# Kernel tuning notes

Hardware: AMD Instinct MI355X
Metric: run time of the kernel (lower is better)

The kernel has to match this reference:

```python
import jax, jax.numpy as jnp
import numpy as np
import math

B, L, IN, HID, NLAYERS, AA = 16, 512, 512, 512, 6, 21
KAPPA_ADD = 5.0


def _sru_layer(x, W, v, b):
    # x: [L, B, din]; W: [din, 2*HID*k]; v, b: [2(gate f/r), 2(dir), HID]
    Lx, Bx, din = x.shape
    d = HID
    k = W.shape[1] // (2 * d)  # 4 if projecting residual, 3 if residual = input
    U = (x @ W).reshape(Lx, Bx, 2, d, k)
    res = U[..., 3] if k == 4 else x.reshape(Lx, Bx, 2, d)
    # time-flip direction 1 so a single scan handles both directions
    flip = lambda a: jnp.concatenate([a[:, :, :1], a[::-1, :, 1:]], axis=2)
    u0, u1, u2, resf = flip(U[..., 0]), flip(U[..., 1]), flip(U[..., 2]), flip(res)
    vf, vr = v[0], v[1]
    bf, br = b[0], b[1]

    def step(c, t):
        u0t, u1t, u2t, rt = t
        f = jax.nn.sigmoid(u1t + vf * c + bf)
        c1 = f * c + (1.0 - f) * u0t
        r = jax.nn.sigmoid(u2t + vr * c1 + br)
        h = r * c1 + (1.0 - r) * rt
        return c1, h

    c0 = jnp.zeros((Bx, 2, d), x.dtype)
    _, H = jax.lax.scan(step, c0, (u0, u1, u2, resf))
    return flip(H).reshape(Lx, Bx, 2 * d)


def setup_inputs():
    key = jax.random.key(0)
    inp = {}
    inp['input'] = jax.random.normal(jax.random.fold_in(key, 0), (B, L, IN), jnp.float32)
    inp['hidden'] = jnp.zeros((NLAYERS, B, 2 * HID), jnp.float32)
    for l in range(NLAYERS):
        din = IN if l == 0 else 2 * HID
        k = 4 if din != 2 * HID else 3
        inp[f'sru_w{l}'] = jax.random.normal(jax.random.fold_in(key, 10 + l), (din, 2 * HID * k), jnp.float32) * (1.0 / math.sqrt(din))
        inp[f'sru_v{l}'] = jax.random.normal(jax.random.fold_in(key, 20 + l), (2, 2, HID), jnp.float32) * 0.1
        inp[f'sru_b{l}'] = jnp.zeros((2, 2, HID), jnp.float32)

    def lin(seed, din, dout):
        w = jax.random.normal(jax.random.fold_in(key, seed), (din, dout), jnp.float32) * (1.0 / math.sqrt(din))
        return w, jnp.zeros((dout,), jnp.float32)

    inp['fc1_logits_w'], inp['fc1_logits_b'] = lin(30, 2 * HID, HID)
    inp['fc2_logits_w'], inp['fc2_logits_b'] = lin(31, HID, AA)
    inp['fc1_angles_w'], inp['fc1_angles_b'] = lin(32, 2 * HID, HID)
    inp['fc2_means_w'], inp['fc2_means_b'] = lin(33, HID, 2)
    inp['fc2_kappas_w'], inp['fc2_kappas_b'] = lin(34, HID, 2)
    return inp


def reference(input, hidden, sru_w0, sru_v0, sru_b0, sru_w1, sru_v1, sru_b1, sru_w2, sru_v2, sru_b2, sru_w3, sru_v3, sru_b3, sru_w4, sru_v4, sru_b4, sru_w5, sru_v5, sru_b5, fc1_logits_w, fc1_logits_b, fc2_logits_w, fc2_logits_b, fc1_angles_w, fc1_angles_b, fc2_means_w, fc2_means_b, fc2_kappas_w, fc2_kappas_b):
    x = input.transpose(1, 0, 2)  # [L, B, IN]
    ws = [sru_w0, sru_w1, sru_w2, sru_w3, sru_w4, sru_w5]
    vs = [sru_v0, sru_v1, sru_v2, sru_v3, sru_v4, sru_v5]
    bs = [sru_b0, sru_b1, sru_b2, sru_b3, sru_b4, sru_b5]
    for W, v, b in zip(ws, vs, bs):
        x = _sru_layer(x, W, v, b)
    sru_out = x.transpose(1, 0, 2)  # [B, L, 2*HID]
    h_log = sru_out @ fc1_logits_w + fc1_logits_b
    output_logits = jax.nn.log_softmax(h_log @ fc2_logits_w + fc2_logits_b, axis=-1)
    h_ang = sru_out @ fc1_angles_w + fc1_angles_b
    output_means = jnp.tanh(h_ang @ fc2_means_w + fc2_means_b) * math.pi
    output_kappas = KAPPA_ADD + jax.nn.softplus(h_ang @ fc2_kappas_w + fc2_kappas_b)
    return (output_logits, output_means, output_kappas)
```

## Files before the change

kernel.cpp:

```cpp
#include <hip/hip_runtime.h>

typedef __attribute__((ext_vector_type(8))) short short8;
typedef __attribute__((ext_vector_type(4))) float f32x4;

__device__ __forceinline__ ushort f2bf(float x) {
  unsigned u = __builtin_bit_cast(unsigned, x);
  u = (u + 0x7fffu + ((u >> 16) & 1u)) >> 16;
  return (ushort)u;
}
__device__ __forceinline__ float bf2f(ushort x) {
  return __builtin_bit_cast(float, ((unsigned)x) << 16);
}

#define AS1CP(p) ((const __attribute__((address_space(1))) unsigned int*)(p))
#define AS3CP(p) ((__attribute__((address_space(3))) unsigned int*)(p))
#define GLDS(g, l, SZ) __builtin_amdgcn_global_load_lds(AS1CP(g), AS3CP(l), SZ, 0, 0)

__global__ __launch_bounds__(256) void k_cvt(const float* __restrict__ in,
                                             ushort* __restrict__ out, int n4) {
  int i = blockIdx.x * 256 + threadIdx.x;
  if (i >= n4) return;
  float4 v = reinterpret_cast<const float4*>(in)[i];
  ushort4 o;
  o.x = f2bf(v.x); o.y = f2bf(v.y); o.z = f2bf(v.z); o.w = f2bf(v.w);
  reinterpret_cast<ushort4*>(out)[i] = o;
}

__global__ __launch_bounds__(256) void k_transpose(const float* __restrict__ W,
                                                   ushort* __restrict__ Wt,
                                                   int N, int K) {
  __shared__ float tile[32][33];
  int bx = blockIdx.x * 32;
  int by = blockIdx.y * 32;
  int tx = threadIdx.x, ty = threadIdx.y;
#pragma unroll
  for (int i = 0; i < 32; i += 8)
    tile[ty + i][tx] = W[(size_t)(by + ty + i) * N + bx + tx];
  __syncthreads();
#pragma unroll
  for (int i = 0; i < 32; i += 8)
    Wt[(size_t)(bx + ty + i) * K + by + tx] = f2bf(tile[tx][ty + i]);
}

template <int KKp>
__global__ __launch_bounds__(256) void k_transpose_sru(const float* __restrict__ W,
                                                       ushort* __restrict__ Wt,
                                                       int N, int K) {
  __shared__ float tile[32][33];
  int bx = blockIdx.x * 32;
  int by = blockIdx.y * 32;
  int tx = threadIdx.x, ty = threadIdx.y;
#pragma unroll
  for (int i = 0; i < 32; i += 8)
    tile[ty + i][tx] = W[(size_t)(by + ty + i) * N + bx + tx];
  __syncthreads();
#pragma unroll
  for (int i = 0; i < 32; i += 8) {
    int c = bx + ty + i;
    int ch = c / KKp, j = c - ch * KKp;
    int nc = j * 1024 + ch;
    Wt[(size_t)nc * K + by + tx] = f2bf(tile[tx][ty + i]);
  }
}

template <int BF16OUT>
__global__ __launch_bounds__(256) void k_gemm(const ushort* __restrict__ A,
                                              const ushort* __restrict__ Bt,
                                              void* __restrict__ Cv,
                                              int K, int N) {
  __shared__ __align__(16) ushort lsA[2][2][4096];
  __shared__ __align__(16) ushort lsB[2][2][4096];
  const int tid = threadIdx.x;
  const int bm = blockIdx.x, bn = blockIdx.y;
  const int w = tid >> 6, l = tid & 63;
  const int wm = (w >> 1) * 64, wn = (w & 1) * 64;
  const int lr = l & 15, lg = l >> 4;
  f32x4 acc[4][4] = {};
  const int srow = tid >> 2;
  const int scol = (((tid & 3) ^ ((srow >> 1) & 3))) * 8;
  const ushort* Ag = A + (size_t)(bm * 128 + srow) * K + scol;
  const ushort* Bg = Bt + (size_t)(bn * 128 + srow) * K + scol;
  const int nt = K >> 6;
  const int rxor = (lr >> 1) & 3;

#define GEMM_ISSUE(SL, KT)                                                  \
  {                                                                         \
    GLDS(Ag + (KT), &lsA[SL][0][w * 512], 16);                              \
    GLDS(Ag + (size_t)64 * K + (KT), &lsA[SL][0][2048 + w * 512], 16);      \
    GLDS(Bg + (KT), &lsB[SL][0][w * 512], 16);                              \
    GLDS(Bg + (size_t)64 * K + (KT), &lsB[SL][0][2048 + w * 512], 16);      \
    GLDS(Ag + (KT) + 32, &lsA[SL][1][w * 512], 16);                         \
    GLDS(Ag + (size_t)64 * K + (KT) + 32, &lsA[SL][1][2048 + w * 512], 16); \
    GLDS(Bg + (KT) + 32, &lsB[SL][1][w * 512], 16);                         \
    GLDS(Bg + (size_t)64 * K + (KT) + 32, &lsB[SL][1][2048 + w * 512], 16); \
  }

  GEMM_ISSUE(0, 0);
  for (int t = 0; t < nt; ++t) {
    const int cur = t & 1;
    if (t + 1 < nt) {
      GEMM_ISSUE(cur ^ 1, (t + 1) * 64);
      asm volatile("s_waitcnt vmcnt(8)" ::: "memory");
    } else {
      asm volatile("s_waitcnt vmcnt(0)" ::: "memory");
    }
    asm volatile("s_barrier" ::: "memory");
#pragma unroll
    for (int kk = 0; kk < 2; ++kk) {
      short8 af[4], bfr[4];
#pragma unroll
      for (int i = 0; i < 4; ++i)
        af[i] = *(const short8*)&lsA[cur][kk][(wm + i * 16 + lr) * 32 + ((lg ^ rxor) * 8)];
#pragma unroll
      for (int j = 0; j < 4; ++j)
        bfr[j] = *(const short8*)&lsB[cur][kk][(wn + j * 16 + lr) * 32 + ((lg ^ rxor) * 8)];
#pragma unroll
      for (int i = 0; i < 4; ++i)
#pragma unroll
        for (int j = 0; j < 4; ++j)
          acc[i][j] = __builtin_amdgcn_mfma_f32_16x16x32_bf16(af[i], bfr[j], acc[i][j], 0, 0, 0);
    }
    asm volatile("s_barrier" ::: "memory");
  }
#undef GEMM_ISSUE
  const size_t cbase = (size_t)(bm * 128 + wm + lg * 4) * N + bn * 128 + wn + lr;
  if (BF16OUT) {
    ushort* Cb = (ushort*)Cv + cbase;
#pragma unroll
    for (int i = 0; i < 4; ++i)
#pragma unroll
      for (int j = 0; j < 4; ++j)
#pragma unroll
        for (int r = 0; r < 4; ++r)
          Cb[(size_t)(i * 16 + r) * N + j * 16] = f2bf(acc[i][j][r]);
  } else {
    float* Cb = (float*)Cv + cbase;
#pragma unroll
    for (int i = 0; i < 4; ++i)
#pragma unroll
      for (int j = 0; j < 4; ++j)
#pragma unroll
        for (int r = 0; r < 4; ++r)
          Cb[(size_t)(i * 16 + r) * N + j * 16] = acc[i][j][r];
  }
}

template <int WRITE_NEXT>
__global__ __launch_bounds__(64, 1) void sru_rec10(const ushort* __restrict__ U,
                                                   const ushort* __restrict__ Rp,
                                                   const float* __restrict__ v,
                                                   const float* __restrict__ bb,
                                                   ushort* __restrict__ H,
                                                   ushort* __restrict__ Hres) {
  const size_t PL = (size_t)1024 * 8192;
  const int lane = threadIdx.x;
  const int blk = blockIdx.x;
  const int b = blk >> 4, cg = blk & 15;
  const int ch = cg * 64 + lane;
  const int dir = ch >> 9;
  const float vf = v[ch], vr = v[1024 + ch];
  const float bfv = bb[ch], brv = bb[1024 + ch];
  const float vfn = -vf, vrn = -vr;
  const float kf0 = -bfv, kr0 = -brv;
  const size_t rowoff = (size_t)ch * 8192 + b * 512;
  const ushort* U0 = U + rowoff;
  const ushort* U1 = U0 + PL;
  const ushort* U2 = U0 + 2 * PL;
  const ushort* Rb = Rp + rowoff;
  ushort* Hb = H + (size_t)b * 512 * 1024 + ch;
  ushort* Hr = Hres + rowoff;

  short8 q0[8], q1[8], q2[8], qr[8];

#define SR_ISSUE(J, TI)                                                        \
  {                                                                            \
    const int tb_ = dir ? (504 - (TI) * 8) : ((TI) * 8);                       \
    q0[J] = *(const short8*)(U0 + tb_);                                        \
    q1[J] = *(const short8*)(U1 + tb_);                                        \
    q2[J] = *(const short8*)(U2 + tb_);                                        \
    qr[J] = *(const short8*)(Rb + tb_);                                        \
  }

#define SR_COMP(J, TI)                                                         \
  {                                                                            \
    const int tb_ = dir ? (504 - (TI) * 8) : ((TI) * 8);                       \
    short8 hv = {};                                                            \
    _Pragma("unroll")                                                          \
    for (int s = 0; s < 8; ++s) {                                              \
      const int e0 = s, e1 = 7 - s;                                            \
      const int e = dir ? e1 : e0;                                             \
      float u0 = bf2f((ushort)(dir ? q0[J][e1] : q0[J][e0]));                  \
      float u1 = bf2f((ushort)(dir ? q1[J][e1] : q1[J][e0]));                  \
      float u2 = bf2f((ushort)(dir ? q2[J][e1] : q2[J][e0]));                  \
      float uR = bf2f((ushort)(dir ? qr[J][e1] : qr[J][e0]));                  \
      float ef = __expf(__builtin_fmaf(vfn, c, kf0 - u1));                     \
      float f = __builtin_amdgcn_rcpf(1.f + ef);                               \
      c = __builtin_fmaf(f, c - u0, u0);                                       \
      float er = __expf(__builtin_fmaf(vrn, c, kr0 - u2));                     \
      float r = __builtin_amdgcn_rcpf(1.f + er);                               \
      float hh = __builtin_fmaf(r, c - uR, uR);                                \
      ushort hb = f2bf(hh);                                                    \
      Hb[(size_t)(tb_ + e) * 1024] = hb;                                       \
      if (WRITE_NEXT) { if (dir) hv[e1] = (short)hb; else hv[e0] = (short)hb; }\
    }                                                                          \
    if (WRITE_NEXT) *(short8*)(Hr + tb_) = hv;                                 \
  }

  SR_ISSUE(0, 0) SR_ISSUE(1, 1) SR_ISSUE(2, 2) SR_ISSUE(3, 3)
  SR_ISSUE(4, 4) SR_ISSUE(5, 5) SR_ISSUE(6, 6)
  float c = 0.f;
#pragma unroll 1
  for (int ii = 0; ii < 7; ++ii) {
#define TILE_J(J)                                                              \
    {                                                                          \
      const int i = ii * 8 + (J);                                              \
      SR_ISSUE((((J) + 7) & 7), i + 7)                                         \
      asm volatile("s_waitcnt vmcnt(28)" ::: "memory");                        \
      SR_COMP(J, i)                                                            \
    }
    TILE_J(0) TILE_J(1) TILE_J(2) TILE_J(3)
    TILE_J(4) TILE_J(5) TILE_J(6) TILE_J(7)
#undef TILE_J
  }
  SR_ISSUE(7, 63)
  asm volatile("s_waitcnt vmcnt(28)" ::: "memory"); SR_COMP(0, 56)
  asm volatile("s_waitcnt vmcnt(24)" ::: "memory"); SR_COMP(1, 57)
  asm volatile("s_waitcnt vmcnt(20)" ::: "memory"); SR_COMP(2, 58)
  asm volatile("s_waitcnt vmcnt(16)" ::: "memory"); SR_COMP(3, 59)
  asm volatile("s_waitcnt vmcnt(12)" ::: "memory"); SR_COMP(4, 60)
  asm volatile("s_waitcnt vmcnt(8)" ::: "memory");  SR_COMP(5, 61)
  asm volatile("s_waitcnt vmcnt(4)" ::: "memory");  SR_COMP(6, 62)
  asm volatile("s_waitcnt vmcnt(0)" ::: "memory");  SR_COMP(7, 63)
#undef SR_ISSUE
#undef SR_COMP
}

__global__ __launch_bounds__(256) void k_buildW2(const float* __restrict__ w2l,
                                                 const float* __restrict__ w2m,
                                                 const float* __restrict__ w2k,
                                                 ushort* __restrict__ Wt2) {
  int i = blockIdx.x * 256 + threadIdx.x;
  if (i >= 128 * 1024) return;
  int n = i >> 10, k = i & 1023;
  float vv = 0.f;
  if (n < 21 && k < 512) vv = w2l[k * 21 + n];
  else if (n >= 21 && n < 23 && k >= 512) vv = w2m[(k - 512) * 2 + (n - 21)];
  else if (n >= 23 && n < 25 && k >= 512) vv = w2k[(k - 512) * 2 + (n - 23)];
  Wt2[i] = f2bf(vv);
}

__global__ __launch_bounds__(64) void k_bias25(const float* __restrict__ b1l,
                                               const float* __restrict__ b1a,
                                               const float* __restrict__ w2l,
                                               const float* __restrict__ b2l,
                                               const float* __restrict__ w2m,
                                               const float* __restrict__ b2m,
                                               const float* __restrict__ w2k,
                                               const float* __restrict__ b2k,
                                               float* __restrict__ b2adj) {
  int o = threadIdx.x;
  if (o >= 25) return;
  float s;
  if (o < 21) {
    s = b2l[o];
    for (int k = 0; k < 512; ++k) s += b1l[k] * w2l[k * 21 + o];
  } else if (o < 23) {
    s = b2m[o - 21];
    for (int k = 0; k < 512; ++k) s += b1a[k] * w2m[k * 2 + (o - 21)];
  } else {
    s = b2k[o - 23];
    for (int k = 0; k < 512; ++k) s += b1a[k] * w2k[k * 2 + (o - 23)];
  }
  b2adj[o] = s;
}

__global__ __launch_bounds__(64) void k_act(const float* __restrict__ T,
                                            const float* __restrict__ b2adj,
                                            float* __restrict__ out) {
  const int row = blockIdx.x;
  const int lane = threadIdx.x;
  float myv = 0.f;
  if (lane < 25) myv = T[(size_t)row * 128 + lane] + b2adj[lane];
  float x = (lane < 21) ? myv : -1e30f;
#pragma unroll
  for (int off = 32; off; off >>= 1) x = fmaxf(x, __shfl_xor(x, off));
  float e = (lane < 21) ? expf(myv - x) : 0.f;
#pragma unroll
  for (int off = 32; off; off >>= 1) e += __shfl_xor(e, off);
  float lse = x + logf(e);
  if (lane < 21) {
    out[(size_t)row * 21 + lane] = myv - lse;
  } else if (lane < 23) {
    out[172032 + row * 2 + (lane - 21)] = tanhf(myv) * 3.14159265358979323846f;
  } else if (lane < 25) {
    float sp = (myv > 20.f) ? myv : log1pf(expf(myv));
    out[188416 + row * 2 + (lane - 23)] = 5.f + sp;
  }
}

extern "C" void kernel_launch(void* const* d_in, const int* in_sizes, int n_in,
                              void* d_out, int out_size, void* d_ws, size_t ws_size,
                              hipStream_t stream) {
  (void)in_sizes; (void)n_in; (void)out_size; (void)ws_size;
  const float* input = (const float*)d_in[0];
  const float* sw[6]; const float* sv[6]; const float* sb[6];
  for (int l = 0; l < 6; ++l) {
    sw[l] = (const float*)d_in[2 + 3 * l];
    sv[l] = (const float*)d_in[3 + 3 * l];
    sb[l] = (const float*)d_in[4 + 3 * l];
  }
  const float* fc1lw = (const float*)d_in[20];
  const float* fc1lb = (const float*)d_in[21];
  const float* fc2lw = (const float*)d_in[22];
  const float* fc2lb = (const float*)d_in[23];
  const float* fc1aw = (const float*)d_in[24];
  const float* fc1ab = (const float*)d_in[25];
  const float* fc2mw = (const float*)d_in[26];
  const float* fc2mb = (const float*)d_in[27];
  const float* fc2kw = (const float*)d_in[28];
  const float* fc2kb = (const float*)d_in[29];

  char* ws = (char*)d_ws;
  ushort* U = (ushort*)ws;
  ushort* Hcat2 = (ushort*)ws;
  float* T = (float*)(ws + 33554432);
  ushort* HresA = (ushort*)(ws + 67108864);
  ushort* HresB = (ushort*)(ws + 83886080);
  ushort* H0 = (ushort*)(ws + 134217728);
  ushort* H1 = (ushort*)(ws + 150994944);
  ushort* X0 = (ushort*)(ws + 167772160);
  const size_t wbase = 176160768;
  ushort* Wtl[6];
  Wtl[0] = (ushort*)(ws + wbase);
  for (int l = 1; l < 6; ++l)
    Wtl[l] = (ushort*)(ws + wbase + 4194304 + (size_t)(l - 1) * 6291456);
  ushort* Wfc = (ushort*)(ws + wbase + 4194304 + 5ull * 6291456);
  ushort* Wt2 = (ushort*)(ws + wbase + 37748736);
  float* b2adj = (float*)(ws + wbase + 38010880);

  k_cvt<<<4096, 256, 0, stream>>>(input, X0, 8192 * 512 / 4);
  k_buildW2<<<512, 256, 0, stream>>>(fc2lw, fc2mw, fc2kw, Wt2);
  k_bias25<<<1, 64, 0, stream>>>(fc1lb, fc1ab, fc2lw, fc2lb, fc2mw, fc2mb,
                                 fc2kw, fc2kb, b2adj);

  k_transpose_sru<4><<<dim3(128, 16), dim3(32, 8), 0, stream>>>(sw[0], Wtl[0], 4096, 512);
  for (int l = 1; l < 6; ++l)
    k_transpose_sru<3><<<dim3(96, 32), dim3(32, 8), 0, stream>>>(sw[l], Wtl[l], 3072, 1024);
  k_transpose<<<dim3(16, 32), dim3(32, 8), 0, stream>>>(fc1lw, Wfc, 512, 1024);
  k_transpose<<<dim3(16, 32), dim3(32, 8), 0, stream>>>(fc1aw, Wfc + (size_t)512 * 1024, 512, 1024);

  const size_t PL = (size_t)1024 * 8192;
  for (int l = 0; l < 6; ++l) {
    const ushort* Ain = (l == 0) ? X0 : ((l & 1) ? H0 : H1);
    ushort* Hout = (l & 1) ? H1 : H0;
    int K = (l == 0) ? 512 : 1024;
    int NF = (l == 0) ? 4096 : 3072;
    k_gemm<1><<<dim3(NF / 128, 64), 256, 0, stream>>>(Wtl[l], Ain, U, K, 8192);
    const ushort* Rp = (l == 0) ? (U + 3 * PL) : ((l & 1) ? HresA : HresB);
    ushort* Hro = (l & 1) ? HresB : HresA;
    if (l < 5)
      sru_rec10<1><<<256, 64, 0, stream>>>(U, Rp, sv[l], sb[l], Hout, Hro);
    else
      sru_rec10<0><<<256, 64, 0, stream>>>(U, Rp, sv[l], sb[l], Hout, Hro);
  }

  k_gemm<1><<<dim3(64, 8), 256, 0, stream>>>(H1, Wfc, Hcat2, 1024, 1024);

  k_gemm<0><<<dim3(64, 1), 256, 0, stream>>>(Hcat2, Wt2, T, 1024, 128);

  k_act<<<8192, 64, 0, stream>>>(T, b2adj, (float*)d_out);
}
```

Baseline: 743.2 us.

## Interleave two channel recurrences per wavefront in SRU scan kernel

```diff
diff --git a/kernel.cpp b/kernel.cpp
--- a/kernel.cpp
+++ b/kernel.cpp
@@ -146,7 +146,7 @@
 }
 
 template <int WRITE_NEXT>
-__global__ __launch_bounds__(64, 1) void sru_rec10(const ushort* __restrict__ U,
+__global__ __launch_bounds__(64, 1) void sru_rec11(const ushort* __restrict__ U,
                                                    const ushort* __restrict__ Rp,
                                                    const float* __restrict__ v,
                                                    const float* __restrict__ bb,
@@ -155,84 +155,97 @@
   const size_t PL = (size_t)1024 * 8192;
   const int lane = threadIdx.x;
   const int blk = blockIdx.x;
-  const int b = blk >> 4, cg = blk & 15;
-  const int ch = cg * 64 + lane;
-  const int dir = ch >> 9;
-  const float vf = v[ch], vr = v[1024 + ch];
-  const float bfv = bb[ch], brv = bb[1024 + ch];
-  const float vfn = -vf, vrn = -vr;
-  const float kf0 = -bfv, kr0 = -brv;
-  const size_t rowoff = (size_t)ch * 8192 + b * 512;
-  const ushort* U0 = U + rowoff;
-  const ushort* U1 = U0 + PL;
-  const ushort* U2 = U0 + 2 * PL;
-  const ushort* Rb = Rp + rowoff;
-  ushort* Hb = H + (size_t)b * 512 * 1024 + ch;
-  ushort* Hr = Hres + rowoff;
-
-  short8 q0[8], q1[8], q2[8], qr[8];
+  const int b = blk >> 3, cg = blk & 7;
+  const int dir = cg >> 2;
+  const int ch0 = cg * 128 + lane;
+  const int ch1 = ch0 + 64;
+  const float vf0 = v[ch0], vr0 = v[1024 + ch0];
+  const float vf1 = v[ch1], vr1 = v[1024 + ch1];
+  const float kf0a = -bb[ch0], kr0a = -bb[1024 + ch0];
+  const float kf0b = -bb[ch1], kr0b = -bb[1024 + ch1];
+  const float vfn0 = -vf0, vrn0 = -vr0, vfn1 = -vf1, vrn1 = -vr1;
+  const size_t ro0 = (size_t)ch0 * 8192 + b * 512;
+  const size_t ro1 = (size_t)ch1 * 8192 + b * 512;
+  const ushort* U0a = U + ro0;       const ushort* U0b = U + ro1;
+  const ushort* U1a = U0a + PL;      const ushort* U1b = U0b + PL;
+  const ushort* U2a = U0a + 2 * PL;  const ushort* U2b = U0b + 2 * PL;
+  const ushort* Ra = Rp + ro0;       const ushort* Rb_ = Rp + ro1;
+  ushort* Hb0 = H + (size_t)b * 512 * 1024 + ch0;
+  ushort* Hb1 = H + (size_t)b * 512 * 1024 + ch1;
+  ushort* Hr0 = Hres + ro0;          ushort* Hr1 = Hres + ro1;
+
+  short8 q0a[4], q1a[4], q2a[4], qra[4];
+  short8 q0b[4], q1b[4], q2b[4], qrb[4];
 
 #define SR_ISSUE(J, TI)                                                        \
   {                                                                            \
     const int tb_ = dir ? (504 - (TI) * 8) : ((TI) * 8);                       \
-    q0[J] = *(const short8*)(U0 + tb_);                                        \
-    q1[J] = *(const short8*)(U1 + tb_);                                        \
-    q2[J] = *(const short8*)(U2 + tb_);                                        \
-    qr[J] = *(const short8*)(Rb + tb_);                                        \
+    q0a[J] = *(const short8*)(U0a + tb_);  q0b[J] = *(const short8*)(U0b + tb_);\
+    q1a[J] = *(const short8*)(U1a + tb_);  q1b[J] = *(const short8*)(U1b + tb_);\
+    q2a[J] = *(const short8*)(U2a + tb_);  q2b[J] = *(const short8*)(U2b + tb_);\
+    qra[J] = *(const short8*)(Ra + tb_);   qrb[J] = *(const short8*)(Rb_ + tb_);\
   }
 
 #define SR_COMP(J, TI)                                                         \
   {                                                                            \
     const int tb_ = dir ? (504 - (TI) * 8) : ((TI) * 8);                       \
-    short8 hv = {};                                                            \
+    short8 hva = {}, hvb = {};                                                 \
     _Pragma("unroll")                                                          \
     for (int s = 0; s < 8; ++s) {                                              \
-      const int e0 = s, e1 = 7 - s;                                            \
-      const int e = dir ? e1 : e0;                                             \
-      float u0 = bf2f((ushort)(dir ? q0[J][e1] : q0[J][e0]));                  \
-      float u1 = bf2f((ushort)(dir ? q1[J][e1] : q1[J][e0]));                  \
-      float u2 = bf2f((ushort)(dir ? q2[J][e1] : q2[J][e0]));                  \
-      float uR = bf2f((ushort)(dir ? qr[J][e1] : qr[J][e0]));                  \
-      float ef = __expf(__builtin_fmaf(vfn, c, kf0 - u1));                     \
-      float f = __builtin_amdgcn_rcpf(1.f + ef);                               \
-      c = __builtin_fmaf(f, c - u0, u0);                                       \
-      float er = __expf(__builtin_fmaf(vrn, c, kr0 - u2));                     \
-      float r = __builtin_amdgcn_rcpf(1.f + er);                               \
-      float hh = __builtin_fmaf(r, c - uR, uR);                                \
-      ushort hb = f2bf(hh);                                                    \
-      Hb[(size_t)(tb_ + e) * 1024] = hb;                                       \
-      if (WRITE_NEXT) { if (dir) hv[e1] = (short)hb; else hv[e0] = (short)hb; }\
+      const int e = dir ? (7 - s) : s;                                         \
+      float u0A = bf2f((ushort)q0a[J][e]), u0B = bf2f((ushort)q0b[J][e]);      \
+      float u1A = bf2f((ushort)q1a[J][e]), u1B = bf2f((ushort)q1b[J][e]);      \
+      float u2A = bf2f((ushort)q2a[J][e]), u2B = bf2f((ushort)q2b[J][e]);      \
+      float uRA = bf2f((ushort)qra[J][e]), uRB = bf2f((ushort)qrb[J][e]);      \
+      float efA = __expf(__builtin_fmaf(vfn0, c0, kf0a - u1A));                \
+      float efB = __expf(__builtin_fmaf(vfn1, c1, kf0b - u1B));                \
+      float fA = __builtin_amdgcn_rcpf(1.f + efA);                             \
+      float fB = __builtin_amdgcn_rcpf(1.f + efB);                             \
+      c0 = __builtin_fmaf(fA, c0 - u0A, u0A);                                  \
+      c1 = __builtin_fmaf(fB, c1 - u0B, u0B);                                  \
+      float erA = __expf(__builtin_fmaf(vrn0, c0, kr0a - u2A));                \
+      float erB = __expf(__builtin_fmaf(vrn1, c1, kr0b - u2B));                \
+      float rA = __builtin_amdgcn_rcpf(1.f + erA);                             \
+      float rB = __builtin_amdgcn_rcpf(1.f + erB);                             \
+      float hhA = __builtin_fmaf(rA, c0 - uRA, uRA);                           \
+      float hhB = __builtin_fmaf(rB, c1 - uRB, uRB);                           \
+      ushort hbA = f2bf(hhA), hbB = f2bf(hhB);                                 \
+      Hb0[(size_t)(tb_ + e) * 1024] = hbA;                                     \
+      Hb1[(size_t)(tb_ + e) * 1024] = hbB;                                     \
+      if (WRITE_NEXT) { hva[e] = (short)hbA; hvb[e] = (short)hbB; }            \
     }                                                                          \
-    if (WRITE_NEXT) *(short8*)(Hr + tb_) = hv;                                 \
-  }
-
-  SR_ISSUE(0, 0) SR_ISSUE(1, 1) SR_ISSUE(2, 2) SR_ISSUE(3, 3)
-  SR_ISSUE(4, 4) SR_ISSUE(5, 5) SR_ISSUE(6, 6)
-  float c = 0.f;
+    if (WRITE_NEXT) { *(short8*)(Hr0 + tb_) = hva; *(short8*)(Hr1 + tb_) = hvb; } \
+  }
+
+#define SR_W(N) asm volatile("s_waitcnt vmcnt(" #N ")" ::: "memory");
+
+  SR_ISSUE(0, 0) SR_ISSUE(1, 1) SR_ISSUE(2, 2)
+  float c0 = 0.f, c1 = 0.f;
+  SR_ISSUE(3, 3)  SR_W(24) SR_COMP(0, 0)
+  SR_ISSUE(0, 4)  SR_W(40) SR_COMP(1, 1)
+  SR_ISSUE(1, 5)  SR_W(56) SR_COMP(2, 2)
+  SR_ISSUE(2, 6)  SR_W(63) SR_COMP(3, 3)
 #pragma unroll 1
-  for (int ii = 0; ii < 7; ++ii) {
+  for (int ii = 1; ii < 15; ++ii) {
 #define TILE_J(J)                                                              \
     {                                                                          \
-      const int i = ii * 8 + (J);                                              \
-      SR_ISSUE((((J) + 7) & 7), i + 7)                                         \
-      asm volatile("s_waitcnt vmcnt(28)" ::: "memory");                        \
+      const int i = ii * 4 + (J);                                              \
+      SR_ISSUE((((J) + 3) & 3), i + 3)                                         \
+      SR_W(63)                                                                 \
       SR_COMP(J, i)                                                            \
     }
     TILE_J(0) TILE_J(1) TILE_J(2) TILE_J(3)
-    TILE_J(4) TILE_J(5) TILE_J(6) TILE_J(7)
 #undef TILE_J
   }
-  SR_ISSUE(7, 63)
-  asm volatile("s_waitcnt vmcnt(28)" ::: "memory"); SR_COMP(0, 56)
-  asm volatile("s_waitcnt vmcnt(24)" ::: "memory"); SR_COMP(1, 57)
-  asm volatile("s_waitcnt vmcnt(20)" ::: "memory"); SR_COMP(2, 58)
-  asm volatile("s_waitcnt vmcnt(16)" ::: "memory"); SR_COMP(3, 59)
-  asm volatile("s_waitcnt vmcnt(12)" ::: "memory"); SR_COMP(4, 60)
-  asm volatile("s_waitcnt vmcnt(8)" ::: "memory");  SR_COMP(5, 61)
-  asm volatile("s_waitcnt vmcnt(4)" ::: "memory");  SR_COMP(6, 62)
-  asm volatile("s_waitcnt vmcnt(0)" ::: "memory");  SR_COMP(7, 63)
+  SR_ISSUE(3, 63)
+  SR_W(63) SR_COMP(0, 60)
+  SR_W(63) SR_COMP(1, 61)
+  SR_W(56) SR_COMP(2, 62)
+  SR_W(48) SR_COMP(3, 63)
+  asm volatile("s_waitcnt vmcnt(0)" ::: "memory");
 #undef SR_ISSUE
 #undef SR_COMP
+#undef SR_W
 }
 
 __global__ __launch_bounds__(256) void k_buildW2(const float* __restrict__ w2l,
@@ -359,9 +372,9 @@
     const ushort* Rp = (l == 0) ? (U + 3 * PL) : ((l & 1) ? HresA : HresB);
     ushort* Hro = (l & 1) ? HresB : HresA;
     if (l < 5)
-      sru_rec10<1><<<256, 64, 0, stream>>>(U, Rp, sv[l], sb[l], Hout, Hro);
+      sru_rec11<1><<<128, 64, 0, stream>>>(U, Rp, sv[l], sb[l], Hout, Hro);
     else
-      sru_rec10<0><<<256, 64, 0, stream>>>(U, Rp, sv[l], sb[l], Hout, Hro);
+      sru_rec11<0><<<128, 64, 0, stream>>>(U, Rp, sv[l], sb[l], Hout, Hro);
   }
 
   k_gemm<1><<<dim3(64, 8), 256, 0, stream>>>(H1, Wfc, Hcat2, 1024, 1024);
```

Measured after the change: 1.494 ms. 101% more time.
